# Performance work log

Measured on AMD Instinct MI355X. Metric: run time of the kernel, lower is better.

Reference implementation:

```python
import jax, jax.numpy as jnp
import numpy as np

D_MODEL = 1024
HEAD_DIM = 128
SEQ_LEN = 4096
BATCH = 4


def setup_inputs() -> dict:
    key = jax.random.key(0)
    kx, kq, kk, kv, ko = jax.random.split(key, 5)
    s = 1.0 / np.sqrt(D_MODEL)
    so = 1.0 / np.sqrt(HEAD_DIM)
    return {
        "x": jax.random.normal(kx, (SEQ_LEN, BATCH, D_MODEL), dtype=jnp.float32),
        "Wq": jax.random.uniform(kq, (HEAD_DIM, D_MODEL), jnp.float32, -s, s),
        "Wk": jax.random.uniform(kk, (HEAD_DIM, D_MODEL), jnp.float32, -s, s),
        "Wv": jax.random.uniform(kv, (HEAD_DIM, D_MODEL), jnp.float32, -s, s),
        "Wo": jax.random.uniform(ko, (D_MODEL, HEAD_DIM), jnp.float32, -so, so),
    }


def reference(x, Wq, Wk, Wv, Wo):
    # x: (S, B, D)
    S = x.shape[0]
    scale = Wq.shape[0] ** (-0.5)  # head_dim ** -0.5
    # Projections (Linear: x @ W.T) -> (B, S, H)
    Q = jnp.einsum('sbd,hd->bsh', x, Wq)
    K = jnp.einsum('sbd,hd->bsh', x, Wk)
    V = jnp.einsum('sbd,hd->bsh', x, Wv)
    scores = jnp.einsum('bqh,bkh->bqk', Q, K) * scale  # (B, S, S)
    causal = jnp.tril(jnp.ones((S, S), dtype=bool))
    scores = jnp.where(causal[None], scores, -jnp.inf)
    attn = jax.nn.softmax(scores, axis=-1)
    attn = jnp.nan_to_num(attn, nan=0.0)
    out = jnp.einsum('bqk,bkh->bqh', attn, V)  # (B, S, H)
    # out_proj then back to (S, B, D)
    return jnp.einsum('bsh,dh->sbd', out, Wo)
```

## Files before the change

kernel.cpp:

```cpp
#include <hip/hip_runtime.h>
#include <hip/hip_bf16.h>

#define S_LEN 4096
#define BATCH 4
#define DMODEL 1024
#define HDIM 128
#define NSLOT 8

typedef __attribute__((ext_vector_type(8))) short short8;
typedef __attribute__((ext_vector_type(4))) short short4v;
typedef __attribute__((ext_vector_type(4))) float float4v;
typedef __attribute__((ext_vector_type(16))) float float16v;
typedef __attribute__((ext_vector_type(4))) int int4v;

#define MASKVAL (-3.0e38f)
#define MINIT   (-1.0e30f)

static __device__ __forceinline__ unsigned short f2bf(float f) {
    __hip_bfloat16 h = __float2bfloat16(f);
    return *reinterpret_cast<unsigned short*>(&h);
}
static __device__ __forceinline__ unsigned short f2h(float f) {
    _Float16 h = (_Float16)f; return *reinterpret_cast<unsigned short*>(&h);
}
static __device__ __forceinline__ float h2f(unsigned short u) {
    _Float16 h = *reinterpret_cast<_Float16*>(&u); return (float)h;
}
static __device__ __forceinline__ short8 ldf(const unsigned short* p) {
    return *reinterpret_cast<const short8*>(p);
}
static __device__ __forceinline__ short8 pack_p(const float* pv, int hi) {
    unsigned int A  = (unsigned int)f2bf(pv[0]) | ((unsigned int)f2bf(pv[1]) << 16);
    unsigned int Bw = (unsigned int)f2bf(pv[2]) | ((unsigned int)f2bf(pv[3]) << 16);
    unsigned int C  = (unsigned int)f2bf(pv[4]) | ((unsigned int)f2bf(pv[5]) << 16);
    unsigned int D  = (unsigned int)f2bf(pv[6]) | ((unsigned int)f2bf(pv[7]) << 16);
    unsigned int y1 = (unsigned int)__shfl_xor((int)(hi ? A : C), 32);
    unsigned int y2 = (unsigned int)__shfl_xor((int)(hi ? Bw : D), 32);
    int4v pw;
    pw[0] = (int)(hi ? y1 : A);
    pw[1] = (int)(hi ? y2 : Bw);
    pw[2] = (int)(hi ? C : y1);
    pw[3] = (int)(hi ? D : y2);
    union { int4v iv; short8 s; } pu; pu.iv = pw;
    return pu.s;
}

__global__ __launch_bounds__(256) void xprep_kernel(
    const float* __restrict__ x, unsigned short* __restrict__ xf)
{
    int n = blockIdx.x * 256 + threadIdx.x;
    int b = n >> 17;
    int rem = n & 131071;
    int sb = rem >> 10;
    int rem2 = rem & 1023;
    int kq = rem2 >> 4;
    int grp = rem2 & 15;
    int lane0 = grp * 4;
    int par = grp >> 3;
    int s0 = lane0 & 31;
    int k = kq * 16 + par * 8;

    short8 hv[4];
#pragma unroll
    for (int r = 0; r < 4; r++) {
        int s = sb * 32 + s0 + r;
        const float* src = &x[((size_t)s * BATCH + b) * DMODEL + k];
        float4 v0 = *reinterpret_cast<const float4*>(src);
        float4 v1 = *reinterpret_cast<const float4*>(src + 4);
        short8 h;
        h[0] = (short)f2bf(v0.x); h[1] = (short)f2bf(v0.y);
        h[2] = (short)f2bf(v0.z); h[3] = (short)f2bf(v0.w);
        h[4] = (short)f2bf(v1.x); h[5] = (short)f2bf(v1.y);
        h[6] = (short)f2bf(v1.z); h[7] = (short)f2bf(v1.w);
        hv[r] = h;
    }
    size_t addr = (((size_t)b * 128 + sb) * 64 + kq) * 512 + (size_t)lane0 * 8;
#pragma unroll
    for (int r = 0; r < 4; r++)
        *reinterpret_cast<short8*>(xf + addr + r * 8) = hv[r];
}

__global__ __launch_bounds__(256) void wprep_kernel(
    const float* __restrict__ Wq, const float* __restrict__ Wk,
    const float* __restrict__ Wv, unsigned short* __restrict__ Wqf,
    unsigned short* __restrict__ Wkf, unsigned short* __restrict__ Wvf)
{
    const int which = blockIdx.y;
    const float* W = (which == 0) ? Wq : (which == 1) ? Wk : Wv;
    unsigned short* Wf = (which == 0) ? Wqf : (which == 1) ? Wkf : Wvf;
    int n = blockIdx.x * 256 + threadIdx.x;
    int d = n >> 7, k8 = n & 127;
    const float* src = &W[(size_t)d * DMODEL + k8 * 8];
    float4 v0 = *reinterpret_cast<const float4*>(src);
    float4 v1 = *reinterpret_cast<const float4*>(src + 4);
    short8 h;
    h[0] = (short)f2bf(v0.x); h[1] = (short)f2bf(v0.y);
    h[2] = (short)f2bf(v0.z); h[3] = (short)f2bf(v0.w);
    h[4] = (short)f2bf(v1.x); h[5] = (short)f2bf(v1.y);
    h[6] = (short)f2bf(v1.z); h[7] = (short)f2bf(v1.w);
    size_t addr = (((size_t)(d >> 5)) * 64 + (k8 >> 1)) * 512
                + (size_t)(((d & 31) + 32 * (k8 & 1)) * 8);
    *reinterpret_cast<short8*>(Wf + addr) = h;
}

__global__ __launch_bounds__(256) void qkv_gemm_kernel(
    const unsigned short* __restrict__ xf, const unsigned short* __restrict__ Wqf,
    const unsigned short* __restrict__ Wkf, const unsigned short* __restrict__ Wvf,
    unsigned short* __restrict__ Qf, unsigned short* __restrict__ Kf,
    unsigned short* __restrict__ Vf)
{
    __shared__ float cacc[2 * 4096];

    const int t = threadIdx.x;
    const int w = t >> 6;
    const int lane = t & 63;
    const int hi = lane >> 5;
    const int tloc = w & 1;
    const int half = w >> 1;
    const int tile = blockIdx.x * 2 + tloc;
    const int which = tile >> 9;
    const int rem = tile & 511;
    const int b = rem >> 7;
    const int sblk = rem & 127;

    const unsigned short* Wf = (which == 0) ? Wqf : (which == 1) ? Wkf : Wvf;
    const unsigned short* xp =
        xf + (((size_t)b * 128 + sblk) * 64 + half * 32) * 512 + lane * 8;
    const unsigned short* wp = Wf + (size_t)half * 32 * 512 + lane * 8;

    float16v acc[4];
#pragma unroll
    for (int i = 0; i < 4; i++)
#pragma unroll
        for (int r = 0; r < 16; r++) acc[i][r] = 0.f;

    {
        short8 xA = ldf(xp);
        short8 wA[4];
#pragma unroll
        for (int d4 = 0; d4 < 4; d4++) wA[d4] = ldf(wp + (size_t)(d4 * 64) * 512);
        for (int ks = 0; ks < 32; ks++) {
            short8 xB = xA;
            short8 wB[4];
#pragma unroll
            for (int d4 = 0; d4 < 4; d4++) wB[d4] = wA[d4];
            if (ks < 31) {
                xB = ldf(xp + (ks + 1) * 512);
#pragma unroll
                for (int d4 = 0; d4 < 4; d4++)
                    wB[d4] = ldf(wp + (size_t)(d4 * 64 + ks + 1) * 512);
            }
            __builtin_amdgcn_s_setprio(1);
            if (which != 2) {
#pragma unroll
                for (int d4 = 0; d4 < 4; d4++)
                    acc[d4] = __builtin_amdgcn_mfma_f32_32x32x16_bf16(
                        wA[d4], xA, acc[d4], 0, 0, 0);
            } else {
#pragma unroll
                for (int d4 = 0; d4 < 4; d4++)
                    acc[d4] = __builtin_amdgcn_mfma_f32_32x32x16_bf16(
                        xA, wA[d4], acc[d4], 0, 0, 0);
            }
            __builtin_amdgcn_s_setprio(0);
            xA = xB;
#pragma unroll
            for (int d4 = 0; d4 < 4; d4++) wA[d4] = wB[d4];
        }
    }

    float* my = cacc + tloc * 4096;
    if (half == 1) {
#pragma unroll
        for (int db = 0; db < 4; db++)
#pragma unroll
            for (int rc = 0; rc < 4; rc++) {
                float4v v;
#pragma unroll
                for (int j = 0; j < 4; j++) v[j] = acc[db][rc * 4 + j];
                *reinterpret_cast<float4v*>(
                    my + (db * 4 + rc) * 256 + lane * 4) = v;
            }
    }
    __syncthreads();
    if (half != 0) return;

#pragma unroll
    for (int db = 0; db < 4; db++)
#pragma unroll
        for (int rc = 0; rc < 4; rc++) {
            float4v v = *reinterpret_cast<const float4v*>(
                my + (db * 4 + rc) * 256 + lane * 4);
#pragma unroll
            for (int j = 0; j < 4; j++) acc[db][rc * 4 + j] += v[j];
        }

    if (which != 2) {
        unsigned short* Of = (which == 0) ? Qf : Kf;
        const float scale = (which == 0) ? 0.08838834764831845f : 1.0f;
#pragma unroll
        for (int db = 0; db < 4; db++)
#pragma unroll
            for (int g = 0; g < 4; g++) {
                int f = db * 2 + (g >> 1);
                size_t addr = (((size_t)b * 128 + sblk) * 8 + f) * 512
                            + (size_t)(((lane & 31) + 32 * (g & 1)) * 8 + 4 * hi);
                short4v ov;
#pragma unroll
                for (int j = 0; j < 4; j++)
                    ov[j] = (short)f2bf(acc[db][g * 4 + j] * scale);
                *reinterpret_cast<short4v*>(Of + addr) = ov;
            }
    } else {
#pragma unroll
        for (int hb = 0; hb < 4; hb++)
#pragma unroll
            for (int g = 0; g < 4; g++) {
                int kt16 = sblk * 2 + (g >> 1);
                size_t addr = (((size_t)b * 256 + kt16) * 4 + hb) * 512
                            + (size_t)(((lane & 31) + 32 * (g & 1)) * 8 + 4 * hi);
                short4v ov;
#pragma unroll
                for (int j = 0; j < 4; j++)
                    ov[j] = (short)f2bf(acc[hb][g * 4 + j]);
                *reinterpret_cast<short4v*>(Vf + addr) = ov;
            }
    }
}

__global__ __launch_bounds__(256) void attn_kernel(
    const unsigned short* __restrict__ Qf, const unsigned short* __restrict__ Kf,
    const unsigned short* __restrict__ Vf, unsigned short* __restrict__ Opart,
    float* __restrict__ Mpart, float* __restrict__ Lpart)
{
    const int t = threadIdx.x;
    const int w = t >> 6;
    const int lane = t & 63;
    const int l31 = lane & 31;
    const int hi = lane >> 5;

    const int i = blockIdx.x;
    const int xx = i & 7;
    const int b = xx >> 1;
    int j = (i >> 3) * 2 + (xx & 1);
    int qt = 31;
    while (true) {
        int cnt = (qt + 4) >> 2;
        if (j < cnt) break;
        j -= cnt; qt--;
    }
    const int c = j;

    const int nkv = 2 * (qt + 1);
    const int lo = c * 8;
    const int hic = min(lo + 8, nkv);

    const int qb = qt * 128;
    const int qrow = qb + w * 32 + l31;
    const int lastblk = (qb + w * 32 + 31) >> 6;
    const int myhi = min(hic, lastblk + 1);

    const unsigned short* qp =
        Qf + (((size_t)b * 128 + (qt * 4 + w)) * 8) * 512 + lane * 8;
    short8 qf[8];
#pragma unroll
    for (int f = 0; f < 8; f++) qf[f] = ldf(qp + f * 512);

    const unsigned short* kbase =
        Kf + (size_t)b * (S_LEN / 32) * 8 * 512 + lane * 8;
    const unsigned short* vbase =
        Vf + (size_t)b * (S_LEN / 16) * 4 * 512 + lane * 8;

    float m_run = MINIT, l_run = 0.f;
    float16v o[4];
#pragma unroll
    for (int hb = 0; hb < 4; hb++)
#pragma unroll
        for (int r = 0; r < 16; r++) o[hb][r] = 0.f;

    short8 kn[4];
    {
        const unsigned short* kp0 = kbase + (size_t)lo * 8192;
#pragma unroll
        for (int jj = 0; jj < 4; jj++) kn[jj] = ldf(kp0 + jj * 512);
    }

    for (int ti = lo; ti < myhi; ti++) {
        const int kvb = ti * 64;
        const unsigned short* kp = kbase + (size_t)ti * 8192;
        const unsigned short* vp = vbase + (size_t)ti * 8192;
        const unsigned short* kpn =
            kbase + (size_t)((ti + 1 < myhi) ? ti + 1 : ti) * 8192;

        short8 ka[4], kb[4], va[4], vb[4];
#pragma unroll
        for (int jj = 0; jj < 4; jj++) kb[jj] = ldf(kp + (4 + jj) * 512);

        float16v s0, s1;
#pragma unroll
        for (int r = 0; r < 16; r++) { s0[r] = 0.f; s1[r] = 0.f; }

        __builtin_amdgcn_s_setprio(1);
#pragma unroll
        for (int jj = 0; jj < 4; jj++)
            s0 = __builtin_amdgcn_mfma_f32_32x32x16_bf16(kn[jj], qf[jj], s0, 0, 0, 0);
        __builtin_amdgcn_s_setprio(0);
#pragma unroll
        for (int jj = 0; jj < 4; jj++) ka[jj] = ldf(kp + 4096 + jj * 512);
        __builtin_amdgcn_s_setprio(1);
#pragma unroll
        for (int jj = 0; jj < 4; jj++)
            s0 = __builtin_amdgcn_mfma_f32_32x32x16_bf16(kb[jj], qf[4 + jj], s0, 0, 0, 0);
        __builtin_amdgcn_s_setprio(0);
#pragma unroll
        for (int jj = 0; jj < 4; jj++) kb[jj] = ldf(kp + 4096 + (4 + jj) * 512);
        __builtin_amdgcn_s_setprio(1);
#pragma unroll
        for (int jj = 0; jj < 4; jj++)
            s1 = __builtin_amdgcn_mfma_f32_32x32x16_bf16(ka[jj], qf[jj], s1, 0, 0, 0);
        __builtin_amdgcn_s_setprio(0);
#pragma unroll
        for (int jj = 0; jj < 4; jj++) va[jj] = ldf(vp + jj * 512);
        __builtin_amdgcn_s_setprio(1);
#pragma unroll
        for (int jj = 0; jj < 4; jj++)
            s1 = __builtin_amdgcn_mfma_f32_32x32x16_bf16(kb[jj], qf[4 + jj], s1, 0, 0, 0);
        __builtin_amdgcn_s_setprio(0);
#pragma unroll
        for (int jj = 0; jj < 4; jj++) vb[jj] = ldf(vp + (4 + jj) * 512);

        if (kvb + 63 > qb + w * 32) {
#pragma unroll
            for (int r = 0; r < 16; r++) {
                int kv0 = kvb + (r & 3) + 8 * (r >> 2) + 4 * hi;
                if (kv0 > qrow) s0[r] = MASKVAL;
                if (kv0 + 32 > qrow) s1[r] = MASKVAL;
            }
        }

        float mx[16];
#pragma unroll
        for (int r = 0; r < 16; r++) mx[r] = fmaxf(s0[r], s1[r]);
#pragma unroll
        for (int st = 8; st >= 1; st >>= 1)
#pragma unroll
            for (int r = 0; r < st; r++) mx[r] = fmaxf(mx[r], mx[r + st]);
        float pmax = fmaxf(mx[0], __shfl_xor(mx[0], 32));
        if (!__all(pmax - m_run <= 8.0f)) {
            float mnew = fmaxf(m_run, pmax);
            float alpha = __expf(m_run - mnew);
            l_run *= alpha;
#pragma unroll
            for (int hb = 0; hb < 4; hb++) o[hb] = o[hb] * alpha;
            m_run = mnew;
        }
#pragma unroll
        for (int r = 0; r < 16; r++) s0[r] = __expf(s0[r] - m_run);
#pragma unroll
        for (int r = 0; r < 16; r++) s1[r] = __expf(s1[r] - m_run);
        float sm[16];
#pragma unroll
        for (int r = 0; r < 16; r++) sm[r] = s0[r] + s1[r];
#pragma unroll
        for (int st = 8; st >= 1; st >>= 1)
#pragma unroll
            for (int r = 0; r < st; r++) sm[r] += sm[r + st];
        l_run += sm[0] + __shfl_xor(sm[0], 32);

        float t0[8], t1[8], t2[8], t3[8];
#pragma unroll
        for (int jj = 0; jj < 8; jj++) { t0[jj] = s0[jj]; t1[jj] = s0[8 + jj]; }
#pragma unroll
        for (int jj = 0; jj < 8; jj++) { t2[jj] = s1[jj]; t3[jj] = s1[8 + jj]; }

#pragma unroll
        for (int jj = 0; jj < 4; jj++) ka[jj] = ldf(vp + (8 + jj) * 512);
        short8 p0 = pack_p(t0, hi);
        __builtin_amdgcn_s_setprio(1);
#pragma unroll
        for (int hb = 0; hb < 4; hb++)
            o[hb] = __builtin_amdgcn_mfma_f32_32x32x16_bf16(va[hb], p0, o[hb], 0, 0, 0);
        __builtin_amdgcn_s_setprio(0);
#pragma unroll
        for (int jj = 0; jj < 4; jj++) kb[jj] = ldf(vp + (12 + jj) * 512);
        short8 p1 = pack_p(t1, hi);
        __builtin_amdgcn_s_setprio(1);
#pragma unroll
        for (int hb = 0; hb < 4; hb++)
            o[hb] = __builtin_amdgcn_mfma_f32_32x32x16_bf16(vb[hb], p1, o[hb], 0, 0, 0);
        __builtin_amdgcn_s_setprio(0);
#pragma unroll
        for (int jj = 0; jj < 4; jj++) kn[jj] = ldf(kpn + jj * 512);
        short8 p2 = pack_p(t2, hi);
        __builtin_amdgcn_s_setprio(1);
#pragma unroll
        for (int hb = 0; hb < 4; hb++)
            o[hb] = __builtin_amdgcn_mfma_f32_32x32x16_bf16(ka[hb], p2, o[hb], 0, 0, 0);
        short8 p3 = pack_p(t3, hi);
#pragma unroll
        for (int hb = 0; hb < 4; hb++)
            o[hb] = __builtin_amdgcn_mfma_f32_32x32x16_bf16(kb[hb], p3, o[hb], 0, 0, 0);
        __builtin_amdgcn_s_setprio(0);
    }

    const size_t R0 = (size_t)(c * BATCH + b) * S_LEN;
    const float inv = (l_run > 0.f) ? 1.f / l_run : 0.f;
#pragma unroll
    for (int hb = 0; hb < 4; hb++)
#pragma unroll
        for (int g = 0; g < 4; g++) {
            int h0 = hb * 32 + g * 8 + hi * 4;
            short4v ov;
#pragma unroll
            for (int jj = 0; jj < 4; jj++)
                ov[jj] = (short)f2h(o[hb][g * 4 + jj] * inv);
            *reinterpret_cast<short4v*>(&Opart[(R0 + qrow) * HDIM + h0]) = ov;
        }
    if (hi == 0) { Mpart[R0 + qrow] = m_run; Lpart[R0 + qrow] = l_run; }
}

__global__ __launch_bounds__(256) void combine_kernel(
    const unsigned short* __restrict__ Opart, const float* __restrict__ Mpart,
    const float* __restrict__ Lpart, unsigned short* __restrict__ Ob)
{
    const int BS = BATCH * S_LEN;
    int idx = blockIdx.x * 256 + threadIdx.x;
    int r = idx >> 4, hc = (idx & 15) * 8;
    int q = r & (S_LEN - 1);
    int qt = q >> 7;
    int nkv = 2 * (qt + 1);
    int cnt = (nkv + 7) >> 3;

    float m = -INFINITY;
    for (int j = 0; j < cnt; j++) m = fmaxf(m, Mpart[j * BS + r]);
    float wsum = 0.f;
    float acc[8];
#pragma unroll
    for (int e = 0; e < 8; e++) acc[e] = 0.f;
    for (int j = 0; j < cnt; j++) {
        float wj = __expf(Mpart[j * BS + r] - m) * Lpart[j * BS + r];
        wsum += wj;
        short8 o = *reinterpret_cast<const short8*>(
            &Opart[((size_t)j * BS + r) * HDIM + hc]);
#pragma unroll
        for (int e = 0; e < 8; e++) acc[e] += wj * h2f((unsigned short)o[e]);
    }
    float inv = 1.f / wsum;
    short8 ob;
#pragma unroll
    for (int e = 0; e < 8; e++) ob[e] = (short)f2bf(acc[e] * inv);
    *reinterpret_cast<short8*>(&Ob[(size_t)r * HDIM + hc]) = ob;
}

__global__ __launch_bounds__(256) void out_proj_kernel(
    const unsigned short* __restrict__ Ob, const float* __restrict__ Wo,
    float* __restrict__ out)
{
    __shared__ unsigned short As[128 * 128];
    __shared__ unsigned short Bs[128 * 128];

    const int t = threadIdx.x;
    const int lane = t & 63, w = t >> 6;
    const int l15 = lane & 15, l4 = lane >> 4;
    const int wr = (w >> 1) * 64, wc = (w & 1) * 64;
    const int s0 = blockIdx.x * 128;
    const int d0 = blockIdx.y * 128;
    const int b = blockIdx.z;

#pragma unroll
    for (int p = 0; p < 8; p++) {
        int e = p * 2048 + t * 8;
        int r = e >> 7, h = e & 127;
        short8 v = *reinterpret_cast<const short8*>(
            &Ob[((size_t)b * S_LEN + s0 + r) * HDIM + h]);
        int off = (r * 256 + h * 2) ^ ((r & 7) << 4);
        *reinterpret_cast<short8*>(reinterpret_cast<char*>(As) + off) = v;
    }
#pragma unroll
    for (int p = 0; p < 16; p++) {
        int e = p * 1024 + t * 4;
        int r = e >> 7, h = e & 127;
        float4 v = *reinterpret_cast<const float4*>(&Wo[(size_t)(d0 + r) * HDIM + h]);
        short4v hh;
        hh[0] = (short)f2bf(v.x); hh[1] = (short)f2bf(v.y);
        hh[2] = (short)f2bf(v.z); hh[3] = (short)f2bf(v.w);
        int off = (r * 256 + h * 2) ^ ((r & 7) << 4);
        *reinterpret_cast<short4v*>(reinterpret_cast<char*>(Bs) + off) = hh;
    }
    __syncthreads();

    float4v acc[4][4];
#pragma unroll
    for (int i = 0; i < 4; i++)
#pragma unroll
        for (int j = 0; j < 4; j++) acc[i][j] = (float4v){0.f, 0.f, 0.f, 0.f};

#pragma unroll
    for (int kk = 0; kk < 4; kk++) {
        short8 a[4], bf[4];
#pragma unroll
        for (int mi = 0; mi < 4; mi++) {
            int row = wr + mi * 16 + l15;
            int off = (row * 256 + (kk * 32 + l4 * 8) * 2) ^ ((row & 7) << 4);
            a[mi] = *reinterpret_cast<const short8*>(
                reinterpret_cast<const char*>(As) + off);
        }
#pragma unroll
        for (int ni = 0; ni < 4; ni++) {
            int row = wc + ni * 16 + l15;
            int off = (row * 256 + (kk * 32 + l4 * 8) * 2) ^ ((row & 7) << 4);
            bf[ni] = *reinterpret_cast<const short8*>(
                reinterpret_cast<const char*>(Bs) + off);
        }
#pragma unroll
        for (int mi = 0; mi < 4; mi++)
#pragma unroll
            for (int ni = 0; ni < 4; ni++)
                acc[mi][ni] = __builtin_amdgcn_mfma_f32_16x16x32_bf16(
                    a[mi], bf[ni], acc[mi][ni], 0, 0, 0);
    }

#pragma unroll
    for (int mi = 0; mi < 4; mi++)
#pragma unroll
        for (int ni = 0; ni < 4; ni++)
#pragma unroll
            for (int r = 0; r < 4; r++) {
                int s = s0 + wr + mi * 16 + l4 * 4 + r;
                int d = d0 + wc + ni * 16 + l15;
                out[((size_t)s * BATCH + b) * DMODEL + d] = acc[mi][ni][r];
            }
}

extern "C" void kernel_launch(void* const* d_in, const int* in_sizes, int n_in,
                              void* d_out, int out_size, void* d_ws, size_t ws_size,
                              hipStream_t stream) {
    const float* x  = (const float*)d_in[0];
    const float* Wq = (const float*)d_in[1];
    const float* Wk = (const float*)d_in[2];
    const float* Wv = (const float*)d_in[3];
    const float* Wo = (const float*)d_in[4];
    float* out = (float*)d_out;

    const size_t BS = (size_t)BATCH * S_LEN;
    unsigned short* xf    = (unsigned short*)d_ws;
    unsigned short* Opart = (unsigned short*)d_ws;
    float* Mpart = (float*)((char*)d_ws + (32u << 20));
    float* Lpart = Mpart + NSLOT * BS;
    unsigned short* Wqf = (unsigned short*)((char*)d_ws + (33u << 20));
    unsigned short* Wkf = Wqf + 131072;
    unsigned short* Wvf = Wkf + 131072;
    unsigned short* Qf  = Wvf + 131072;
    unsigned short* Kf  = Qf + 2097152;
    unsigned short* Vf  = Kf + 2097152;
    unsigned short* Ob  = Vf + 2097152;

    xprep_kernel<<<2048, 256, 0, stream>>>(x, xf);
    wprep_kernel<<<dim3(64, 3), 256, 0, stream>>>(Wq, Wk, Wv, Wqf, Wkf, Wvf);
    qkv_gemm_kernel<<<768, 256, 0, stream>>>(xf, Wqf, Wkf, Wvf, Qf, Kf, Vf);
    attn_kernel<<<576, 256, 0, stream>>>(Qf, Kf, Vf, Opart, Mpart, Lpart);
    combine_kernel<<<1024, 256, 0, stream>>>(Opart, Mpart, Lpart, Ob);
    out_proj_kernel<<<dim3(32, 8, BATCH), 256, 0, stream>>>(Ob, Wo, out);
}
```

Before: 123.7 us.

## Share K/V tiles across waves via double-buffered LDS with global_load_lds

The attention kernel now stages each 64-row K and V tile once per block into double-buffered shared memory using direct global-to-LDS loads, with the next tile prefetched while the current one is consumed. Previously each of the four waves loaded the full K/V tile into its own registers. The aim is to cut redundant global/L2 traffic fourfold and free registers. In exchange it adds a block-wide barrier per tile, drops the interleaved load/MFMA scheduling, and removes the per-wave causal early exit, so some waves do extra fully masked tiles.

```diff
diff --git a/kernel.cpp b/kernel.cpp
--- a/kernel.cpp
+++ b/kernel.cpp
@@ -28,6 +28,12 @@
 }
 static __device__ __forceinline__ short8 ldf(const unsigned short* p) {
     return *reinterpret_cast<const short8*>(p);
+}
+static __device__ __forceinline__ void gll16(const unsigned short* g,
+                                             unsigned short* l) {
+    __builtin_amdgcn_global_load_lds(
+        (const __attribute__((address_space(1))) unsigned int*)g,
+        (__attribute__((address_space(3))) unsigned int*)l, 16, 0, 0);
 }
 static __device__ __forceinline__ short8 pack_p(const float* pv, int hi) {
     unsigned int A  = (unsigned int)f2bf(pv[0]) | ((unsigned int)f2bf(pv[1]) << 16);
@@ -233,6 +239,9 @@
     const unsigned short* __restrict__ Vf, unsigned short* __restrict__ Opart,
     float* __restrict__ Mpart, float* __restrict__ Lpart)
 {
+    __shared__ unsigned short Kb2[2][8192];
+    __shared__ unsigned short Vb2[2][8192];
+
     const int t = threadIdx.x;
     const int w = t >> 6;
     const int lane = t & 63;
@@ -257,8 +266,6 @@
 
     const int qb = qt * 128;
     const int qrow = qb + w * 32 + l31;
-    const int lastblk = (qb + w * 32 + 31) >> 6;
-    const int myhi = min(hic, lastblk + 1);
 
     const unsigned short* qp =
         Qf + (((size_t)b * 128 + (qt * 4 + w)) * 8) * 512 + lane * 8;
@@ -278,56 +285,48 @@
 #pragma unroll
         for (int r = 0; r < 16; r++) o[hb][r] = 0.f;
 
-    short8 kn[4];
     {
-        const unsigned short* kp0 = kbase + (size_t)lo * 8192;
-#pragma unroll
-        for (int jj = 0; jj < 4; jj++) kn[jj] = ldf(kp0 + jj * 512);
-    }
-
-    for (int ti = lo; ti < myhi; ti++) {
+        const unsigned short* kg = kbase + (size_t)lo * 8192;
+        const unsigned short* vg = vbase + (size_t)lo * 8192;
+#pragma unroll
+        for (int jj = 0; jj < 4; jj++) {
+            int fi = 4 * w + jj;
+            gll16(kg + fi * 512, &Kb2[0][fi * 512]);
+            gll16(vg + fi * 512, &Vb2[0][fi * 512]);
+        }
+    }
+    __syncthreads();
+
+    int cur = 0;
+    for (int ti = lo; ti < hic; ti++) {
         const int kvb = ti * 64;
-        const unsigned short* kp = kbase + (size_t)ti * 8192;
-        const unsigned short* vp = vbase + (size_t)ti * 8192;
-        const unsigned short* kpn =
-            kbase + (size_t)((ti + 1 < myhi) ? ti + 1 : ti) * 8192;
-
-        short8 ka[4], kb[4], va[4], vb[4];
-#pragma unroll
-        for (int jj = 0; jj < 4; jj++) kb[jj] = ldf(kp + (4 + jj) * 512);
+        if (ti + 1 < hic) {
+            const unsigned short* kg = kbase + (size_t)(ti + 1) * 8192;
+            const unsigned short* vg = vbase + (size_t)(ti + 1) * 8192;
+#pragma unroll
+            for (int jj = 0; jj < 4; jj++) {
+                int fi = 4 * w + jj;
+                gll16(kg + fi * 512, &Kb2[cur ^ 1][fi * 512]);
+                gll16(vg + fi * 512, &Vb2[cur ^ 1][fi * 512]);
+            }
+        }
+
+        const unsigned short* Kl = &Kb2[cur][0] + lane * 8;
+        const unsigned short* Vl = &Vb2[cur][0] + lane * 8;
 
         float16v s0, s1;
 #pragma unroll
         for (int r = 0; r < 16; r++) { s0[r] = 0.f; s1[r] = 0.f; }
-
         __builtin_amdgcn_s_setprio(1);
 #pragma unroll
-        for (int jj = 0; jj < 4; jj++)
-            s0 = __builtin_amdgcn_mfma_f32_32x32x16_bf16(kn[jj], qf[jj], s0, 0, 0, 0);
+        for (int f = 0; f < 8; f++)
+            s0 = __builtin_amdgcn_mfma_f32_32x32x16_bf16(
+                ldf(Kl + f * 512), qf[f], s0, 0, 0, 0);
+#pragma unroll
+        for (int f = 0; f < 8; f++)
+            s1 = __builtin_amdgcn_mfma_f32_32x32x16_bf16(
+                ldf(Kl + (8 + f) * 512), qf[f], s1, 0, 0, 0);
         __builtin_amdgcn_s_setprio(0);
-#pragma unroll
-        for (int jj = 0; jj < 4; jj++) ka[jj] = ldf(kp + 4096 + jj * 512);
-        __builtin_amdgcn_s_setprio(1);
-#pragma unroll
-        for (int jj = 0; jj < 4; jj++)
-            s0 = __builtin_amdgcn_mfma_f32_32x32x16_bf16(kb[jj], qf[4 + jj], s0, 0, 0, 0);
-        __builtin_amdgcn_s_setprio(0);
-#pragma unroll
-        for (int jj = 0; jj < 4; jj++) kb[jj] = ldf(kp + 4096 + (4 + jj) * 512);
-        __builtin_amdgcn_s_setprio(1);
-#pragma unroll
-        for (int jj = 0; jj < 4; jj++)
-            s1 = __builtin_amdgcn_mfma_f32_32x32x16_bf16(ka[jj], qf[jj], s1, 0, 0, 0);
-        __builtin_amdgcn_s_setprio(0);
-#pragma unroll
-        for (int jj = 0; jj < 4; jj++) va[jj] = ldf(vp + jj * 512);
-        __builtin_amdgcn_s_setprio(1);
-#pragma unroll
-        for (int jj = 0; jj < 4; jj++)
-            s1 = __builtin_amdgcn_mfma_f32_32x32x16_bf16(kb[jj], qf[4 + jj], s1, 0, 0, 0);
-        __builtin_amdgcn_s_setprio(0);
-#pragma unroll
-        for (int jj = 0; jj < 4; jj++) vb[jj] = ldf(vp + (4 + jj) * 512);
 
         if (kvb + 63 > qb + w * 32) {
 #pragma unroll
@@ -373,34 +372,31 @@
 #pragma unroll
         for (int jj = 0; jj < 8; jj++) { t2[jj] = s1[jj]; t3[jj] = s1[8 + jj]; }
 
-#pragma unroll
-        for (int jj = 0; jj < 4; jj++) ka[jj] = ldf(vp + (8 + jj) * 512);
         short8 p0 = pack_p(t0, hi);
         __builtin_amdgcn_s_setprio(1);
 #pragma unroll
         for (int hb = 0; hb < 4; hb++)
-            o[hb] = __builtin_amdgcn_mfma_f32_32x32x16_bf16(va[hb], p0, o[hb], 0, 0, 0);
+            o[hb] = __builtin_amdgcn_mfma_f32_32x32x16_bf16(
+                ldf(Vl + (0 * 4 + hb) * 512), p0, o[hb], 0, 0, 0);
+        short8 p1 = pack_p(t1, hi);
+#pragma unroll
+        for (int hb = 0; hb < 4; hb++)
+            o[hb] = __builtin_amdgcn_mfma_f32_32x32x16_bf16(
+                ldf(Vl + (1 * 4 + hb) * 512), p1, o[hb], 0, 0, 0);
+        short8 p2 = pack_p(t2, hi);
+#pragma unroll
+        for (int hb = 0; hb < 4; hb++)
+            o[hb] = __builtin_amdgcn_mfma_f32_32x32x16_bf16(
+                ldf(Vl + (2 * 4 + hb) * 512), p2, o[hb], 0, 0, 0);
+        short8 p3 = pack_p(t3, hi);
+#pragma unroll
+        for (int hb = 0; hb < 4; hb++)
+            o[hb] = __builtin_amdgcn_mfma_f32_32x32x16_bf16(
+                ldf(Vl + (3 * 4 + hb) * 512), p3, o[hb], 0, 0, 0);
         __builtin_amdgcn_s_setprio(0);
-#pragma unroll
-        for (int jj = 0; jj < 4; jj++) kb[jj] = ldf(vp + (12 + jj) * 512);
-        short8 p1 = pack_p(t1, hi);
-        __builtin_amdgcn_s_setprio(1);
-#pragma unroll
-        for (int hb = 0; hb < 4; hb++)
-            o[hb] = __builtin_amdgcn_mfma_f32_32x32x16_bf16(vb[hb], p1, o[hb], 0, 0, 0);
-        __builtin_amdgcn_s_setprio(0);
-#pragma unroll
-        for (int jj = 0; jj < 4; jj++) kn[jj] = ldf(kpn + jj * 512);
-        short8 p2 = pack_p(t2, hi);
-        __builtin_amdgcn_s_setprio(1);
-#pragma unroll
-        for (int hb = 0; hb < 4; hb++)
-            o[hb] = __builtin_amdgcn_mfma_f32_32x32x16_bf16(ka[hb], p2, o[hb], 0, 0, 0);
-        short8 p3 = pack_p(t3, hi);
-#pragma unroll
-        for (int hb = 0; hb < 4; hb++)
-            o[hb] = __builtin_amdgcn_mfma_f32_32x32x16_bf16(kb[hb], p3, o[hb], 0, 0, 0);
-        __builtin_amdgcn_s_setprio(0);
+
+        __syncthreads();
+        cur ^= 1;
     }
 
     const size_t R0 = (size_t)(c * BATCH + b) * S_LEN;
```

New measurement: 122.7 us. Within noise of the previous version (-0.8%).
